# Optimization experiments

Hardware: AMD Instinct MI355X
Metric: run time of the kernel (lower is better)

The kernel has to match this reference:

```python
import jax, jax.numpy as jnp
import numpy as np

F = 64    # input features
H = 3     # hidden units (hardcoded in the original module)
B = 2048  # batch
T = 512   # timesteps


def setup_inputs() -> dict:
    key = jax.random.key(0)
    ks = jax.random.split(key, 6)
    x = jax.random.normal(ks[0], (B, T, F), dtype=jnp.float32)
    # Keras LSTM kernels: kernel [F, 4H], recurrent_kernel [H, 4H], bias [4H]
    # glorot_uniform scale for kernel
    lim_k = float(np.sqrt(6.0 / (F + 4 * H)))
    W = jax.random.uniform(ks[1], (F, 4 * H), minval=-lim_k, maxval=lim_k, dtype=jnp.float32)
    lim_u = float(np.sqrt(6.0 / (H + 4 * H)))
    U = jax.random.uniform(ks[2], (H, 4 * H), minval=-lim_u, maxval=lim_u, dtype=jnp.float32)
    # Keras default LSTM bias: zeros with forget-gate bias = 1 (unit_forget_bias=True)
    b = jnp.zeros((4 * H,), dtype=jnp.float32).at[H:2 * H].set(1.0)
    lim_d = float(np.sqrt(6.0 / (H + 1)))
    Wd = jax.random.uniform(ks[3], (H, 1), minval=-lim_d, maxval=lim_d, dtype=jnp.float32)
    bd = 0.05 * jax.random.normal(ks[4], (1,), dtype=jnp.float32)  # truncated_normal init
    return {"x": x, "W": W, "U": U, "b": b, "Wd": Wd, "bd": bd}


def _lstm_last_h(x, W, U, b):
    # x: [B, T, F] -> scan over time; gate order in Keras: i, f, g(c), o
    Bsz = x.shape[0]
    h0 = jnp.zeros((Bsz, H), dtype=x.dtype)
    c0 = jnp.zeros((Bsz, H), dtype=x.dtype)

    def step(carry, xt):
        h, c = carry
        z = xt @ W + h @ U + b                     # [B, 4H]
        i = jax.nn.sigmoid(z[:, 0 * H:1 * H])
        f = jax.nn.sigmoid(z[:, 1 * H:2 * H])
        g = jnp.tanh(z[:, 2 * H:3 * H])
        o = jax.nn.sigmoid(z[:, 3 * H:4 * H])
        c_new = f * c + i * g
        h_new = o * jnp.tanh(c_new)
        return (h_new, c_new), None

    (hT, _), _ = jax.lax.scan(step, (h0, c0), jnp.swapaxes(x, 0, 1))  # [T, B, F]
    return hT  # [B, H]


def reference(x, W, U, b, Wd, bd):
    hT = _lstm_last_h(x, W, U, b)
    return jax.nn.sigmoid(hT @ Wd + bd)  # [B, 1]
```

## Files before the change

kernel.cpp:

```cpp
#include <hip/hip_runtime.h>
#include <hip/hip_bf16.h>
#include <cstdint>

#define B_SZ 2048
#define T_SZ 512
#define F_SZ 64
#define BPB  4
#define TCH  32
#define NCHK (T_SZ / TCH)
#define NBLK (B_SZ / BPB)
#define NTHR 256
#define ROWS (BPB * TCH)
#define MT   (ROWS / 16)
#define NPC  (ROWS * 16)
#define NSTG 128
#define PPT  (NPC / NSTG)
#define TSTR 84
#define ESTR 20

#define L2E 1.4426950408889634f

typedef __attribute__((ext_vector_type(8))) short short8;
typedef __attribute__((ext_vector_type(4))) float f32x4;

__device__ __forceinline__ float fast_rcp(float x) { return __builtin_amdgcn_rcpf(x); }
__device__ __forceinline__ float exp2h(float x)    { return __builtin_amdgcn_exp2f(x); }
__device__ __forceinline__ float sigm_s(float zs)  { return fast_rcp(1.0f + exp2h(zs)); }
__device__ __forceinline__ float sigm_n(float x)   { return sigm_s(x * (-L2E)); }

__device__ __forceinline__ unsigned short f2bf(float f) {
    __hip_bfloat16 h = (__hip_bfloat16)f;
    return *reinterpret_cast<unsigned short*>(&h);
}

template<int CTRL>
__device__ __forceinline__ float dppmv(float v) {
    return __int_as_float(__builtin_amdgcn_mov_dpp(__float_as_int(v), CTRL, 0xF, 0xF, true));
}
#define DPP_SHR6 0x116
#define DPP_SHR3 0x113
#define DPP_SHL3 0x103
#define DPP_NB6  0x156
#define DPP_NB7  0x157
#define DPP_NB8  0x158

__global__ __launch_bounds__(NTHR) void lstm_mfma(const float* __restrict__ x,
                                                  const float* __restrict__ W,
                                                  const float* __restrict__ U,
                                                  const float* __restrict__ bias,
                                                  const float* __restrict__ Wd,
                                                  const float* __restrict__ bdp,
                                                  float* __restrict__ out) {
    __shared__ unsigned int xfrag[2][MT * 2 * 256];
    __shared__ float zbuf[2][TCH * TSTR];

    const int tid = threadIdx.x;
    const int wv  = tid >> 6;
    const int ln  = tid & 63;
    const int b0  = blockIdx.x * BPB;

    const int n  = ln & 15;
    const int q  = n / 3;
    const float scq = (q == 2) ? (-2.0f * L2E) : (-L2E);

    short8 bfrag[2];
    #pragma unroll
    for (int kt = 0; kt < 2; ++kt) {
        short8 s;
        #pragma unroll
        for (int e = 0; e < 8; ++e) {
            const int hh = e >> 2, j = e & 3;
            const int kk = kt * 32 + hh * 16 + 4 * (ln >> 4) + j;
            const float w = (n < 12 && wv == 1) ? W[kk * 12 + n] * scq : 0.0f;
            s[e] = (short)f2bf(w);
        }
        bfrag[kt] = s;
    }
    const float bias_s = (n < 12) ? bias[n] * scq : 0.0f;

    const int e16 = ln >> 4;
    float u0 = 0.f, u1 = 0.f, u2 = 0.f, gA = 0.f, gB = 0.f;
    if (n < 12) {
        u0 = U[0 * 12 + n] * scq;
        u1 = U[1 * 12 + n] * scq;
        u2 = U[2 * 12 + n] * scq;
        if (q == 2) { gA = -4.0f * L2E; gB = 2.0f * L2E; }
        else        { gA = 1.0f;        gB = 0.0f;       }
    }
    float cs = 0.f, h0b = 0.f, h1b = 0.f, h2b = 0.f;

    auto comp = [&](float z4) {
        const float z  = fmaf(h0b, u0, fmaf(h1b, u1, fmaf(h2b, u2, z4)));
        const float r  = fast_rcp(1.0f + exp2h(z));
        const float gt = fmaf(gA, r, gB);
        const float iV = dppmv<DPP_SHR6>(gt);
        const float fV = dppmv<DPP_SHR3>(gt);
        const float oV = dppmv<DPP_SHL3>(gt);
        cs = fmaf(fV, cs, iV * gt);
        const float th = fmaf(2.0f, fast_rcp(1.0f + exp2h(cs)), -1.0f);
        const float h  = oV * th;
        h0b = dppmv<DPP_NB6>(h);
        h1b = dppmv<DPP_NB7>(h);
        h2b = dppmv<DPP_NB8>(h);
    };

    auto scan32 = [&](const float* zb) {
        const float* zp = zb + e16 * ESTR + n;
        float pf[8];
        #pragma unroll
        for (int i = 0; i < 8; ++i) pf[i] = zp[i * TSTR];
        __builtin_amdgcn_s_setprio(1);
        #pragma unroll
        for (int tt = 0; tt < TCH; ++tt) {
            const float z4 = pf[tt & 7];
            if (tt + 8 < TCH) pf[tt & 7] = zp[(tt + 8) * TSTR];
            comp(z4);
        }
        __builtin_amdgcn_s_setprio(0);
    };

    float4 v[PPT];
    const int stid = tid - 128;
    auto stage_issue = [&](int ck) {
        const int t0 = ck * TCH;
        #pragma unroll
        for (int i = 0; i < PPT; ++i) {
            const int piece = i * NSTG + stid;
            const int row = piece >> 4, g = piece & 15;
            v[i] = *reinterpret_cast<const float4*>(
                x + ((size_t)(b0 + (row >> 5)) * T_SZ + (t0 + (row & 31))) * F_SZ + (g << 2));
        }
    };
    auto stage_write = [&](int buf) {
        #pragma unroll
        for (int i = 0; i < PPT; ++i) {
            const int piece = i * NSTG + stid;
            const int row = piece >> 4, g = piece & 15;
            const int u_off = ((row >> 4) * 2 + (g >> 3)) * 256
                            + (((row & 15) | ((g & 3) << 4)) << 2) + ((g >> 2) & 1) * 2;
            uint2 pk;
            pk.x = (unsigned)f2bf(v[i].x) | ((unsigned)f2bf(v[i].y) << 16);
            pk.y = (unsigned)f2bf(v[i].z) | ((unsigned)f2bf(v[i].w) << 16);
            *reinterpret_cast<uint2*>(&xfrag[buf][u_off]) = pk;
        }
    };

    auto mfma_chunk = [&](int cur) {
        #pragma unroll
        for (int mt = 0; mt < MT; ++mt) {
            f32x4 acc = { bias_s, bias_s, bias_s, bias_s };
            const short8 a0 = *reinterpret_cast<const short8*>(&xfrag[cur][(mt * 2 + 0) * 256 + (ln << 2)]);
            const short8 a1 = *reinterpret_cast<const short8*>(&xfrag[cur][(mt * 2 + 1) * 256 + (ln << 2)]);
            acc = __builtin_amdgcn_mfma_f32_16x16x32_bf16(a0, bfrag[0], acc, 0, 0, 0);
            acc = __builtin_amdgcn_mfma_f32_16x16x32_bf16(a1, bfrag[1], acc, 0, 0, 0);
            const int rbase = mt * 16 + 4 * (ln >> 4);
            #pragma unroll
            for (int r = 0; r < 4; ++r) {
                const int rr = rbase + r;
                zbuf[cur][(rr & 31) * TSTR + (rr >> 5) * ESTR + n] = acc[r];
            }
        }
    };

    if (wv >= 2) { stage_issue(0); stage_write(0); }
    __syncthreads();

    for (int k = 0; k < NCHK; ++k) {
        const int cur = k & 1;
        if (wv >= 2) {
            if (k + 1 < NCHK) { stage_issue(k + 1); stage_write(cur ^ 1); }
        } else if (wv == 1) {
            mfma_chunk(cur);
        } else if (k > 0) {
            scan32(zbuf[cur ^ 1]);
        }
        __syncthreads();
    }

    if (wv == 0) {
        scan32(zbuf[(NCHK - 1) & 1]);
        if (n == 0) {
            const float logit = bdp[0] + h0b * Wd[0] + h1b * Wd[1] + h2b * Wd[2];
            out[b0 + e16] = sigm_n(logit);
        }
    }
}

extern "C" void kernel_launch(void* const* d_in, const int* in_sizes, int n_in,
                              void* d_out, int out_size, void* d_ws, size_t ws_size,
                              hipStream_t stream) {
    (void)in_sizes; (void)n_in; (void)out_size; (void)d_ws; (void)ws_size;
    const float* x  = (const float*)d_in[0];
    const float* W  = (const float*)d_in[1];
    const float* U  = (const float*)d_in[2];
    const float* b  = (const float*)d_in[3];
    const float* Wd = (const float*)d_in[4];
    const float* bd = (const float*)d_in[5];
    float* out = (float*)d_out;

    lstm_mfma<<<NBLK, NTHR, 0, stream>>>(x, W, U, b, Wd, bd, out);
}
```

Baseline: 54.19 us.

## Scan 64 timesteps every other period using a four-chunk z ring buffer

The z buffer grows from a double buffer to a four-chunk ring. The recurrent scan wave now runs every second period over two chunks (64 steps) instead of 32 steps every period. The aim is to halve the number of scan start-ups and prefetch refills on the serial critical path. In exchange LDS use grows. The scan wave also sits idle on odd periods while the workgroup-wide barrier still forces lockstep, so the serial scan may spread less evenly across periods.

```diff
diff --git a/kernel.cpp b/kernel.cpp
--- a/kernel.cpp
+++ b/kernel.cpp
@@ -52,7 +52,7 @@
                                                   const float* __restrict__ bdp,
                                                   float* __restrict__ out) {
     __shared__ unsigned int xfrag[2][MT * 2 * 256];
-    __shared__ float zbuf[2][TCH * TSTR];
+    __shared__ float zbuf[4 * TCH * TSTR];
 
     const int tid = threadIdx.x;
     const int wv  = tid >> 6;
@@ -104,16 +104,16 @@
         h2b = dppmv<DPP_NB8>(h);
     };
 
-    auto scan32 = [&](const float* zb) {
-        const float* zp = zb + e16 * ESTR + n;
+    auto scan64 = [&](int base_row) {
+        const float* zp = zbuf + (size_t)base_row * TSTR + e16 * ESTR + n;
         float pf[8];
         #pragma unroll
         for (int i = 0; i < 8; ++i) pf[i] = zp[i * TSTR];
         __builtin_amdgcn_s_setprio(1);
         #pragma unroll
-        for (int tt = 0; tt < TCH; ++tt) {
+        for (int tt = 0; tt < 2 * TCH; ++tt) {
             const float z4 = pf[tt & 7];
-            if (tt + 8 < TCH) pf[tt & 7] = zp[(tt + 8) * TSTR];
+            if (tt + 8 < 2 * TCH) pf[tt & 7] = zp[(tt + 8) * TSTR];
             comp(z4);
         }
         __builtin_amdgcn_s_setprio(0);
@@ -145,19 +145,21 @@
         }
     };
 
-    auto mfma_chunk = [&](int cur) {
+    auto mfma_period = [&](int p) {
+        const int buf  = p & 1;
+        const int qoff = (p & 3) * TCH;
         #pragma unroll
         for (int mt = 0; mt < MT; ++mt) {
             f32x4 acc = { bias_s, bias_s, bias_s, bias_s };
-            const short8 a0 = *reinterpret_cast<const short8*>(&xfrag[cur][(mt * 2 + 0) * 256 + (ln << 2)]);
-            const short8 a1 = *reinterpret_cast<const short8*>(&xfrag[cur][(mt * 2 + 1) * 256 + (ln << 2)]);
+            const short8 a0 = *reinterpret_cast<const short8*>(&xfrag[buf][(mt * 2 + 0) * 256 + (ln << 2)]);
+            const short8 a1 = *reinterpret_cast<const short8*>(&xfrag[buf][(mt * 2 + 1) * 256 + (ln << 2)]);
             acc = __builtin_amdgcn_mfma_f32_16x16x32_bf16(a0, bfrag[0], acc, 0, 0, 0);
             acc = __builtin_amdgcn_mfma_f32_16x16x32_bf16(a1, bfrag[1], acc, 0, 0, 0);
             const int rbase = mt * 16 + 4 * (ln >> 4);
             #pragma unroll
             for (int r = 0; r < 4; ++r) {
                 const int rr = rbase + r;
-                zbuf[cur][(rr & 31) * TSTR + (rr >> 5) * ESTR + n] = acc[r];
+                zbuf[(size_t)(qoff + (rr & 31)) * TSTR + (rr >> 5) * ESTR + n] = acc[r];
             }
         }
     };
@@ -165,20 +167,19 @@
     if (wv >= 2) { stage_issue(0); stage_write(0); }
     __syncthreads();
 
-    for (int k = 0; k < NCHK; ++k) {
-        const int cur = k & 1;
+    for (int p = 0; p < NCHK; ++p) {
         if (wv >= 2) {
-            if (k + 1 < NCHK) { stage_issue(k + 1); stage_write(cur ^ 1); }
+            if (p + 1 < NCHK) { stage_issue(p + 1); stage_write((p + 1) & 1); }
         } else if (wv == 1) {
-            mfma_chunk(cur);
-        } else if (k > 0) {
-            scan32(zbuf[cur ^ 1]);
+            mfma_period(p);
+        } else if (p >= 2 && (p & 1) == 0) {
+            scan64(((p - 2) & 3) * TCH);
         }
         __syncthreads();
     }
 
     if (wv == 0) {
-        scan32(zbuf[(NCHK - 1) & 1]);
+        scan64(2 * TCH);
         if (n == 0) {
             const float logit = bdp[0] + h0b * Wd[0] + h1b * Wd[1] + h2b * Wd[2];
             out[b0 + e16] = sigm_n(logit);
```

After: 67.05 us. 23.7% more time.
